# Kernel optimization log

Measured on AMD Instinct MI355X. Metric: run time of the kernel, lower is better.

## Reference

```python
import jax, jax.numpy as jnp
import numpy as np

D_IN = 2048
D_OUT = 2048
SEQ = 4096


def setup_inputs() -> dict:
    key = jax.random.key(0)
    kx, kq, kk, kv = jax.random.split(key, 4)
    x = jax.random.normal(kx, (SEQ, D_IN), dtype=jnp.float32)
    # torch.nn.Linear weights have shape [d_out, d_in]
    s = 1.0 / np.sqrt(D_IN)
    W_q = jax.random.uniform(kq, (D_OUT, D_IN), jnp.float32, -s, s)
    W_k = jax.random.uniform(kk, (D_OUT, D_IN), jnp.float32, -s, s)
    W_v = jax.random.uniform(kv, (D_OUT, D_IN), jnp.float32, -s, s)
    return {"x": x, "W_q": W_q, "W_k": W_k, "W_v": W_v}


def reference(x, W_q, W_k, W_v):
    # projections (torch Linear: x @ W.T)
    q = x @ W_q.T  # [S, D]
    k = x @ W_k.T
    v = x @ W_v.T
    scores = q @ k.T  # [S, S]
    scale = jnp.asarray(k.shape[-1], scores.dtype) ** 0.5
    attn = jax.nn.softmax(scores / scale, axis=-1)
    # post-softmax causal mask + row renormalization (faithful to source)
    S = scores.shape[0]
    mask = jnp.tril(jnp.ones((S, S), dtype=attn.dtype))
    masked = attn * mask
    masked = masked / masked.sum(axis=1, keepdims=True)
    return masked @ v  # [S, D]
```

## Files before the change

kernel.cpp:

```cpp
#include <hip/hip_runtime.h>
#include <hip/hip_bf16.h>
#include <math.h>


typedef __attribute__((ext_vector_type(8))) short bf16x8;
typedef __attribute__((ext_vector_type(4))) float f32x4;
typedef __attribute__((ext_vector_type(8))) unsigned short u16x8;
typedef __attribute__((ext_vector_type(4))) int iv4;

__device__ __forceinline__ unsigned short f2bf(float f) {
  unsigned int u = __float_as_uint(f);
  u += 0x7FFFu + ((u >> 16) & 1u);
  return (unsigned short)(u >> 16);
}

__device__ __forceinline__ void gload16(const unsigned short* g, unsigned short* l) {
  __builtin_amdgcn_global_load_lds(
      (const __attribute__((address_space(1))) void*)g,
      (__attribute__((address_space(3))) void*)l,
      16, 0, 0);
}

template <int OFF>
__device__ __forceinline__ bf16x8 dsr(unsigned addr) {
  iv4 r;
  asm volatile("ds_read_b128 %0, %1 offset:%2" : "=v"(r) : "v"(addr), "i"(OFF));
  return __builtin_bit_cast(bf16x8, r);
}

__global__ void cvt_f32_bf16(const float* __restrict__ in,
                             unsigned short* __restrict__ out, int n) {
  int i = (blockIdx.x * 256 + threadIdx.x) * 8;
  if (i >= n) return;
  float4 a = *(const float4*)(in + i);
  float4 b = *(const float4*)(in + i + 4);
  u16x8 r;
  r[0] = f2bf(a.x); r[1] = f2bf(a.y); r[2] = f2bf(a.z); r[3] = f2bf(a.w);
  r[4] = f2bf(b.x); r[5] = f2bf(b.y); r[6] = f2bf(b.z); r[7] = f2bf(b.w);
  *(u16x8*)(out + i) = r;
}

#define LGKM_SB()                                         \
  asm volatile("s_waitcnt lgkmcnt(0)" ::: "memory");      \
  __builtin_amdgcn_sched_barrier(0)

#define QMFMA(MB, NB, AF, BV)                                                 \
  _Pragma("unroll")                                                           \
  for (int _fm = 0; _fm < 4; ++_fm)                                           \
    _Pragma("unroll")                                                         \
    for (int _fn = 0; _fn < 2; ++_fn)                                         \
      _Pragma("unroll")                                                       \
      for (int _ks = 0; _ks < 2; ++_ks)                                       \
        acc[(MB) + _fm][(NB) + _fn] = __builtin_amdgcn_mfma_f32_16x16x32_bf16( \
            AF[_fm * 2 + _ks], BV[_fn * 2 + _ks], acc[(MB) + _fm][(NB) + _fn], \
            0, 0, 0);

#define STG_A(mhv, tau, bufv)                                                 \
  do {                                                                        \
    unsigned short* _d = lds + (bufv) * 32768 + (mhv) * 8192 + w * 512;       \
    gload16(pA + (size_t)((mhv) * 64) * KC + ((size_t)(tau) << 6), _d);       \
    gload16(pA + (size_t)(128 + (mhv) * 64) * KC + ((size_t)(tau) << 6),      \
            _d + 4096);                                                       \
  } while (0)

#define STG_B(nhv, tau, bufv)                                                 \
  do {                                                                        \
    unsigned short* _d = lds + (bufv) * 32768 + 16384 + (nhv) * 8192 + w * 512;\
    gload16(pB + (size_t)((nhv) * 32) * KC + ((size_t)(tau) << 6), _d);       \
    gload16(pB + (size_t)(128 + (nhv) * 32) * KC + ((size_t)(tau) << 6),      \
            _d + 4096);                                                       \
  } while (0)

template <int KC>
__device__ __forceinline__ void gemm_core(const unsigned short* __restrict__ Ab,
                                          const unsigned short* __restrict__ Bb,
                                          unsigned short* lds, int ktiles,
                                          f32x4 (&acc)[8][4]) {
  const int tid  = threadIdx.x;
  const int lane = tid & 63;
  const int w    = tid >> 6;
  const int wm   = w >> 2;
  const int wn   = w & 3;

  const int base  = w * 8 + (lane >> 3);
  const int gslot = (lane & 7) ^ ((lane >> 3) & 7);
  const unsigned short* pA = Ab + (size_t)base * KC + gslot * 8;
  const unsigned short* pB =
      Bb + (size_t)((base >> 5) * 64 + (base & 31)) * KC + gslot * 8;

  const unsigned lb = (unsigned)(size_t)&lds[0];
  const int rl = lane & 15, g = lane >> 4;
  const unsigned sw0 = (unsigned)(((0 + g) ^ (rl & 7)) * 16);
  const unsigned sw1 = (unsigned)(((4 + g) ^ (rl & 7)) * 16);
  const unsigned rA = lb + (unsigned)(wm * 8192 + rl * 128);
  const unsigned rB = lb + (unsigned)(wn * 4096 + rl * 128);

#pragma unroll
  for (int m = 0; m < 8; ++m)
#pragma unroll
    for (int n = 0; n < 4; ++n) acc[m][n] = f32x4{0.f, 0.f, 0.f, 0.f};

  STG_A(0, 0, 0); STG_B(0, 0, 0); STG_A(1, 0, 0); STG_B(1, 0, 0);
  STG_A(0, 1, 1); STG_B(0, 1, 1); STG_A(1, 1, 1);
  asm volatile("s_waitcnt vmcnt(6)" ::: "memory");
  __builtin_amdgcn_s_barrier();

  for (int t = 0; t < ktiles; ++t) {
    const unsigned bo = (unsigned)(t & 1) << 16;
    const int buf = t & 1, nb = (t + 1) & 1;
    const unsigned aA0 = rA + bo + sw0, aA1 = rA + bo + sw1;
    const unsigned aB0 = rB + bo + sw0, aB1 = rB + bo + sw1;
    bf16x8 af0[8], af1[8], bv0[4], bv1[4];
    af0[0] = dsr<0>(aA0);     af0[1] = dsr<0>(aA1);
    af0[2] = dsr<2048>(aA0);  af0[3] = dsr<2048>(aA1);
    af0[4] = dsr<4096>(aA0);  af0[5] = dsr<4096>(aA1);
    af0[6] = dsr<6144>(aA0);  af0[7] = dsr<6144>(aA1);
    bv0[0] = dsr<32768>(aB0); bv0[1] = dsr<32768>(aB1);
    bv0[2] = dsr<34816>(aB0); bv0[3] = dsr<34816>(aB1);
    if (t + 1 < ktiles) STG_B(1, t + 1, nb);
    __builtin_amdgcn_s_barrier();
    LGKM_SB();
    __builtin_amdgcn_s_setprio(1);
    QMFMA(0, 0, af0, bv0);
    __builtin_amdgcn_s_setprio(0);
    __builtin_amdgcn_s_barrier();
    af1[0] = dsr<16384>(aA0); af1[1] = dsr<16384>(aA1);
    af1[2] = dsr<18432>(aA0); af1[3] = dsr<18432>(aA1);
    af1[4] = dsr<20480>(aA0); af1[5] = dsr<20480>(aA1);
    af1[6] = dsr<22528>(aA0); af1[7] = dsr<22528>(aA1);
    if (t + 2 < ktiles) STG_A(0, t + 2, buf);
    __builtin_amdgcn_s_barrier();
    LGKM_SB();
    __builtin_amdgcn_s_setprio(1);
    QMFMA(4, 0, af1, bv0);
    __builtin_amdgcn_s_setprio(0);
    __builtin_amdgcn_s_barrier();
    bv1[0] = dsr<49152>(aB0); bv1[1] = dsr<49152>(aB1);
    bv1[2] = dsr<51200>(aB0); bv1[3] = dsr<51200>(aB1);
    if (t + 2 < ktiles) STG_B(0, t + 2, buf);
    __builtin_amdgcn_s_barrier();
    LGKM_SB();
    __builtin_amdgcn_s_setprio(1);
    QMFMA(0, 2, af0, bv1);
    __builtin_amdgcn_s_setprio(0);
    __builtin_amdgcn_s_barrier();
    if (t + 2 < ktiles) STG_A(1, t + 2, buf);
    __builtin_amdgcn_s_barrier();
    LGKM_SB();
    __builtin_amdgcn_s_setprio(1);
    QMFMA(4, 2, af1, bv1);
    __builtin_amdgcn_s_setprio(0);
    if (t < ktiles - 2)       { asm volatile("s_waitcnt vmcnt(6)" ::: "memory"); }
    else if (t == ktiles - 2) { asm volatile("s_waitcnt vmcnt(0)" ::: "memory"); }
    __builtin_amdgcn_s_barrier();
  }
}

__device__ __forceinline__ void ep_f32(float* C, const f32x4 (&acc)[8][4],
                                       int r0, int c0, int ldc, float scale) {
  const int lane = threadIdx.x & 63, w = threadIdx.x >> 6;
  const int crow0 = r0 + (w >> 2) * 128 + ((lane >> 4) << 2);
  const int ccol0 = c0 + (w & 3) * 64 + (lane & 15);
#pragma unroll
  for (int m = 0; m < 8; ++m)
#pragma unroll
    for (int n = 0; n < 4; ++n)
#pragma unroll
      for (int j = 0; j < 4; ++j)
        C[(size_t)(crow0 + m * 16 + j) * ldc + (ccol0 + n * 16)] =
            acc[m][n][j] * scale;
}

__device__ __forceinline__ void ep_f32_at(float* C, const f32x4 (&acc)[8][4],
                                          int r0, int c0, int ldc, float scale) {
  const int lane = threadIdx.x & 63, w = threadIdx.x >> 6;
  const int crow0 = r0 + (w >> 2) * 128 + ((lane >> 4) << 2);
  const int ccol0 = c0 + (w & 3) * 64 + (lane & 15);
#pragma unroll
  for (int m = 0; m < 8; ++m)
#pragma unroll
    for (int n = 0; n < 4; ++n)
#pragma unroll
      for (int j = 0; j < 4; ++j)
        atomicAdd(&C[(size_t)(crow0 + m * 16 + j) * ldc + (ccol0 + n * 16)],
                  acc[m][n][j] * scale);
}

__device__ __forceinline__ void ep_bf16(unsigned short* C, const f32x4 (&acc)[8][4],
                                        int r0, int c0, int ldc) {
  const int lane = threadIdx.x & 63, w = threadIdx.x >> 6;
  const int crow0 = r0 + (w >> 2) * 128 + ((lane >> 4) << 2);
  const int ccol0 = c0 + (w & 3) * 64 + (lane & 15);
#pragma unroll
  for (int m = 0; m < 8; ++m)
#pragma unroll
    for (int n = 0; n < 4; ++n)
#pragma unroll
      for (int j = 0; j < 4; ++j)
        C[(size_t)(crow0 + m * 16 + j) * ldc + (ccol0 + n * 16)] =
            f2bf(acc[m][n][j]);
}

__global__ __launch_bounds__(512, 2)
void proj_qk(const unsigned short* __restrict__ xb,
             const unsigned short* __restrict__ wqb,
             const unsigned short* __restrict__ wkb,
             unsigned short* __restrict__ Q, unsigned short* __restrict__ Kb) {
  __shared__ __align__(16) unsigned short lds[65536];
  const int bid = blockIdx.x;
  const int wg = (bid & 7) * 32 + (bid >> 3);
  const int bm = wg >> 4, bnr = wg & 15;
  const unsigned short* B = (bnr < 8) ? wqb : wkb;
  unsigned short* C = (bnr < 8) ? Q : Kb;
  const int bnl = bnr & 7;
  f32x4 acc[8][4];
  gemm_core<2048>(xb + (size_t)bm * 256 * 2048, B + (size_t)bnl * 256 * 2048,
                  lds, 32, acc);
  ep_bf16(C, acc, bm * 256, bnl * 256, 2048);
}

__global__ __launch_bounds__(512, 2)
void vt_qkt(const unsigned short* __restrict__ Qp,
            const unsigned short* __restrict__ Kp,
            const unsigned short* __restrict__ wvb,
            const unsigned short* __restrict__ xb,
            float* __restrict__ sc, unsigned short* __restrict__ Vt,
            float scale) {
  __shared__ __align__(16) unsigned short lds[65536];
  const int id = blockIdx.x;
  f32x4 acc[8][4];
  if (id < 64) {
    const int p = id >> 2, c = id & 3;
    const size_t koff = (size_t)c * 8 * 64;
    gemm_core<2048>(Qp + (size_t)15 * 256 * 2048 + koff,
                    Kp + (size_t)p * 256 * 2048 + koff, lds, 8, acc);
    ep_f32_at(sc, acc, 3840, p * 256, 4096, scale);
  } else if (id < 184) {
    const int q = id - 64;
    int bm = 0;
    while ((bm + 1) * (bm + 2) / 2 <= q) ++bm;
    const int bn = q - bm * (bm + 1) / 2;
    gemm_core<2048>(Qp + (size_t)bm * 256 * 2048,
                    Kp + (size_t)bn * 256 * 2048, lds, 32, acc);
    ep_f32(sc, acc, bm * 256, bn * 256, 4096, scale);
  } else {
    const int v = id - 184, bm = v >> 4, bn = v & 15;
    gemm_core<2048>(wvb + (size_t)bm * 256 * 2048,
                    xb + (size_t)bn * 256 * 2048, lds, 32, acc);
    ep_bf16(Vt, acc, bm * 256, bn * 256, 4096);
  }
}

__global__ __launch_bounds__(512, 2)
void pv(const unsigned short* __restrict__ P,
        const unsigned short* __restrict__ Vt, float* __restrict__ out,
        float* __restrict__ aux) {
  __shared__ __align__(16) unsigned short lds[65536];
  const int id = blockIdx.x;
  const int j = id >> 1, h = id & 1;
  const int bm = j >> 3, bn = j & 7;
  const int kt = (bm + 1) * 4;
  const int k0 = h ? (kt >> 1) : 0;
  const int ktl = h ? (kt - (kt >> 1)) : (kt >> 1);
  f32x4 acc[8][4];
  gemm_core<4096>(P + (size_t)bm * 256 * 4096 + (size_t)k0 * 64,
                  Vt + (size_t)bn * 256 * 4096 + (size_t)k0 * 64, lds, ktl, acc);
  if (h) ep_f32(aux, acc, bm * 256, bn * 256, 2048, 1.0f);
  else   ep_f32(out, acc, bm * 256, bn * 256, 2048, 1.0f);
}

__global__ void add_f32(float* __restrict__ out, const float* __restrict__ aux,
                        int n) {
  int i = (blockIdx.x * 256 + threadIdx.x) * 8;
  if (i >= n) return;
  float4 a0 = *(const float4*)(out + i), a1 = *(const float4*)(out + i + 4);
  float4 b0 = *(const float4*)(aux + i), b1 = *(const float4*)(aux + i + 4);
  a0.x += b0.x; a0.y += b0.y; a0.z += b0.z; a0.w += b0.w;
  a1.x += b1.x; a1.y += b1.y; a1.z += b1.z; a1.w += b1.w;
  *(float4*)(out + i) = a0; *(float4*)(out + i + 4) = a1;
}

__global__ void softmax_causal(const float* __restrict__ Sc,
                               unsigned short* __restrict__ P, int S) {
  const int i = blockIdx.x;
  const int tid = threadIdx.x;
  const int nvalid = i + 1;
  const int pad_end = ((i >> 8) + 1) << 8;
  const float* row = Sc + (size_t)i * S;

  float v[16];
  float m = -1e30f;
#pragma unroll
  for (int it = 0; it < 16; ++it) {
    const int j = tid + it * 256;
    const float x = (j < nvalid) ? row[j] : -1e30f;
    v[it] = x;
    m = fmaxf(m, x);
  }
#pragma unroll
  for (int d = 1; d < 64; d <<= 1) m = fmaxf(m, __shfl_xor(m, d));
  __shared__ float red_m[4], red_s[4];
  const int lane = tid & 63, wv = tid >> 6;
  if (lane == 0) red_m[wv] = m;
  __syncthreads();
  m = fmaxf(fmaxf(red_m[0], red_m[1]), fmaxf(red_m[2], red_m[3]));

  float s = 0.0f;
#pragma unroll
  for (int it = 0; it < 16; ++it) {
    const int j = tid + it * 256;
    const float e = (j < nvalid) ? __expf(v[it] - m) : 0.0f;
    v[it] = e;
    s += e;
  }
#pragma unroll
  for (int d = 1; d < 64; d <<= 1) s += __shfl_xor(s, d);
  if (lane == 0) red_s[wv] = s;
  __syncthreads();
  s = red_s[0] + red_s[1] + red_s[2] + red_s[3];

  const float inv = 1.0f / s;
  unsigned short* prow = P + (size_t)i * S;
#pragma unroll
  for (int it = 0; it < 16; ++it) {
    const int j = tid + it * 256;
    if (j < pad_end) prow[j] = (j < nvalid) ? f2bf(v[it] * inv) : (unsigned short)0;
  }
}

extern "C" void kernel_launch(void* const* d_in, const int* in_sizes, int n_in,
                              void* d_out, int out_size, void* d_ws, size_t ws_size,
                              hipStream_t stream) {
  const float* x  = (const float*)d_in[0];
  const float* Wq = (const float*)d_in[1];
  const float* Wk = (const float*)d_in[2];
  const float* Wv = (const float*)d_in[3];
  float* out = (float*)d_out;

  const int S = 4096, D = 2048;
  char* ws = (char*)d_ws;
  const size_t MB = 1u << 20;
  float*          sc  = (float*)ws;
  float*          aux = (float*)ws;
  unsigned short* xb  = (unsigned short*)(ws + 64 * MB);
  unsigned short* wqb = (unsigned short*)(ws + 80 * MB);
  unsigned short* wkb = (unsigned short*)(ws + 88 * MB);
  unsigned short* wvb = (unsigned short*)(ws + 96 * MB);
  unsigned short* Q   = (unsigned short*)(ws + 104 * MB);
  unsigned short* Kb  = (unsigned short*)(ws + 120 * MB);
  unsigned short* Vt  = (unsigned short*)(ws + 80 * MB);
  unsigned short* P   = (unsigned short*)(ws + 104 * MB);

  cvt_f32_bf16<<<(S * D) / (256 * 8), 256, 0, stream>>>(x, xb, S * D);
  cvt_f32_bf16<<<(D * D) / (256 * 8), 256, 0, stream>>>(Wq, wqb, D * D);
  cvt_f32_bf16<<<(D * D) / (256 * 8), 256, 0, stream>>>(Wk, wkb, D * D);
  cvt_f32_bf16<<<(D * D) / (256 * 8), 256, 0, stream>>>(Wv, wvb, D * D);

  proj_qk<<<256, 512, 0, stream>>>(xb, wqb, wkb, Q, Kb);

  hipMemsetAsync(sc + (size_t)3840 * 4096, 0, (size_t)256 * 4096 * 4, stream);

  const float scale = 1.0f / sqrtf((float)D);
  vt_qkt<<<312, 512, 0, stream>>>(Q, Kb, wvb, xb, sc, Vt, scale);

  softmax_causal<<<S, 256, 0, stream>>>(sc, P, S);

  pv<<<256, 512, 0, stream>>>(P, Vt, out, aux);
  add_f32<<<(S * D) / (256 * 8), 256, 0, stream>>>(out, aux, S * D);
}
```

Baseline: 246.7 us.

## Software-pipeline LDS fragment reads across k-tiles and cut barriers in GEMM core

Restructures the GEMM main loop so the next tile's A/B fragments are read from LDS during the current tile's last MFMA phases, with a prologue that preloads the first tile. Global-to-LDS stages are regrouped and each phase waits on vmcnt(8), or vmcnt(0) at the tail, before a single barrier, which drops roughly half the s_barriers per iteration. The aim is to hide LDS read latency behind MFMA work and reduce synchronization stalls. The price is more live fragment registers and subtler buffer-reuse ordering, which could raise register pressure or create hazards.

```diff
diff --git a/kernel.cpp b/kernel.cpp
--- a/kernel.cpp
+++ b/kernel.cpp
@@ -71,6 +71,12 @@
             _d + 4096);                                                       \
   } while (0)
 
+#define VM_WAIT()                                                             \
+  do {                                                                        \
+    if (tail) { asm volatile("s_waitcnt vmcnt(0)" ::: "memory"); }            \
+    else      { asm volatile("s_waitcnt vmcnt(8)" ::: "memory"); }            \
+  } while (0)
+
 template <int KC>
 __device__ __forceinline__ void gemm_core(const unsigned short* __restrict__ Ab,
                                           const unsigned short* __restrict__ Bb,
@@ -101,57 +107,80 @@
     for (int n = 0; n < 4; ++n) acc[m][n] = f32x4{0.f, 0.f, 0.f, 0.f};
 
   STG_A(0, 0, 0); STG_B(0, 0, 0); STG_A(1, 0, 0); STG_B(1, 0, 0);
-  STG_A(0, 1, 1); STG_B(0, 1, 1); STG_A(1, 1, 1);
-  asm volatile("s_waitcnt vmcnt(6)" ::: "memory");
+  if (ktiles > 1) {
+    STG_A(0, 1, 1); STG_B(0, 1, 1); STG_A(1, 1, 1);
+    asm volatile("s_waitcnt vmcnt(6)" ::: "memory");
+  } else {
+    asm volatile("s_waitcnt vmcnt(0)" ::: "memory");
+  }
   __builtin_amdgcn_s_barrier();
 
-  for (int t = 0; t < ktiles; ++t) {
-    const unsigned bo = (unsigned)(t & 1) << 16;
-    const int buf = t & 1, nb = (t + 1) & 1;
-    const unsigned aA0 = rA + bo + sw0, aA1 = rA + bo + sw1;
-    const unsigned aB0 = rB + bo + sw0, aB1 = rB + bo + sw1;
-    bf16x8 af0[8], af1[8], bv0[4], bv1[4];
+  bf16x8 af0[8], af1[8], bv0[4], bv1[4];
+  {
+    const unsigned aA0 = rA + sw0, aA1 = rA + sw1;
+    const unsigned aB0 = rB + sw0, aB1 = rB + sw1;
     af0[0] = dsr<0>(aA0);     af0[1] = dsr<0>(aA1);
     af0[2] = dsr<2048>(aA0);  af0[3] = dsr<2048>(aA1);
     af0[4] = dsr<4096>(aA0);  af0[5] = dsr<4096>(aA1);
     af0[6] = dsr<6144>(aA0);  af0[7] = dsr<6144>(aA1);
     bv0[0] = dsr<32768>(aB0); bv0[1] = dsr<32768>(aB1);
     bv0[2] = dsr<34816>(aB0); bv0[3] = dsr<34816>(aB1);
-    if (t + 1 < ktiles) STG_B(1, t + 1, nb);
-    __builtin_amdgcn_s_barrier();
+  }
+
+  for (int t = 0; t < ktiles; ++t) {
+    const unsigned bo  = (unsigned)(t & 1) << 16;
+    const unsigned bon = (unsigned)((t + 1) & 1) << 16;
+    const int buf = t & 1, nb = (t + 1) & 1;
+    const bool s1 = (t + 1) < ktiles, s2 = (t + 2) < ktiles;
+    const bool tail = t >= ktiles - 2;
+    const unsigned aA0 = rA + bo + sw0, aA1 = rA + bo + sw1;
+    const unsigned aB0 = rB + bo + sw0, aB1 = rB + bo + sw1;
+    const unsigned nA0 = rA + bon + sw0, nA1 = rA + bon + sw1;
+    const unsigned nB0 = rB + bon + sw0, nB1 = rB + bon + sw1;
+
     LGKM_SB();
     __builtin_amdgcn_s_setprio(1);
     QMFMA(0, 0, af0, bv0);
     __builtin_amdgcn_s_setprio(0);
-    __builtin_amdgcn_s_barrier();
     af1[0] = dsr<16384>(aA0); af1[1] = dsr<16384>(aA1);
     af1[2] = dsr<18432>(aA0); af1[3] = dsr<18432>(aA1);
     af1[4] = dsr<20480>(aA0); af1[5] = dsr<20480>(aA1);
     af1[6] = dsr<22528>(aA0); af1[7] = dsr<22528>(aA1);
-    if (t + 2 < ktiles) STG_A(0, t + 2, buf);
+    if (s1) STG_B(1, t + 1, nb);
+    VM_WAIT();
     __builtin_amdgcn_s_barrier();
+
     LGKM_SB();
     __builtin_amdgcn_s_setprio(1);
     QMFMA(4, 0, af1, bv0);
     __builtin_amdgcn_s_setprio(0);
-    __builtin_amdgcn_s_barrier();
     bv1[0] = dsr<49152>(aB0); bv1[1] = dsr<49152>(aB1);
     bv1[2] = dsr<51200>(aB0); bv1[3] = dsr<51200>(aB1);
-    if (t + 2 < ktiles) STG_B(0, t + 2, buf);
+    if (s2) { STG_A(0, t + 2, buf); STG_B(0, t + 2, buf); }
+    VM_WAIT();
     __builtin_amdgcn_s_barrier();
+
     LGKM_SB();
     __builtin_amdgcn_s_setprio(1);
     QMFMA(0, 2, af0, bv1);
     __builtin_amdgcn_s_setprio(0);
+    if (s1) {
+      af0[0] = dsr<0>(nA0);     af0[1] = dsr<0>(nA1);
+      af0[2] = dsr<2048>(nA0);  af0[3] = dsr<2048>(nA1);
+      af0[4] = dsr<4096>(nA0);  af0[5] = dsr<4096>(nA1);
+      af0[6] = dsr<6144>(nA0);  af0[7] = dsr<6144>(nA1);
+      bv0[0] = dsr<32768>(nB0); bv0[1] = dsr<32768>(nB1);
+      bv0[2] = dsr<34816>(nB0); bv0[3] = dsr<34816>(nB1);
+    }
+    if (s2) STG_A(1, t + 2, buf);
+    VM_WAIT();
     __builtin_amdgcn_s_barrier();
-    if (t + 2 < ktiles) STG_A(1, t + 2, buf);
-    __builtin_amdgcn_s_barrier();
-    LGKM_SB();
+
+    __builtin_amdgcn_sched_barrier(0);
     __builtin_amdgcn_s_setprio(1);
     QMFMA(4, 2, af1, bv1);
     __builtin_amdgcn_s_setprio(0);
-    if (t < ktiles - 2)       { asm volatile("s_waitcnt vmcnt(6)" ::: "memory"); }
-    else if (t == ktiles - 2) { asm volatile("s_waitcnt vmcnt(0)" ::: "memory"); }
+    VM_WAIT();
     __builtin_amdgcn_s_barrier();
   }
 }
```

Result: faster. 240.0 us (-2.7%).
